# Performance work log

Hardware: AMD Instinct MI355X
Metric: run time of the kernel (lower is better)

## Reference

```python
import jax, jax.numpy as jnp
import numpy as np

EPS = 1e-5

def _bn2d(x, gamma, beta):
    # training-mode BatchNorm2d: stats over (B, T, F) per channel, biased var
    m = x.mean(axis=(0, 2, 3), keepdims=True)
    v = x.var(axis=(0, 2, 3), keepdims=True)
    return (x - m) * jax.lax.rsqrt(v + EPS) * gamma[None, :, None, None] + beta[None, :, None, None]

def _gn1(x, gamma, beta):
    # GroupNorm(num_groups=1) on (B, C, T): stats over (C, T) per sample
    m = x.mean(axis=(1, 2), keepdims=True)
    v = x.var(axis=(1, 2), keepdims=True)
    return (x - m) * jax.lax.rsqrt(v + EPS) * gamma[None, :, None] + beta[None, :, None]

def _nearest(x, size):
    # torch F.interpolate(mode='nearest') on last dim: src = floor(dst * L_in / L_out)
    L = x.shape[-1]
    idx = jnp.floor(jnp.arange(size) * (L / size)).astype(jnp.int32)
    return x[..., idx]


def setup_inputs() -> dict:
    key = jax.random.key(0)
    ks = jax.random.split(key, 16)
    B, Ca, T, Fa = 2, 512, 256, 128
    Tv = 64
    d = {
        "audio": jax.random.normal(ks[0], (B, Ca, T, Fa), dtype=jnp.float32),
        "video_emb": jax.random.normal(ks[1], (B, Ca, Tv), dtype=jnp.float32),
        # value_conv: depthwise 1x1 Conv2d (no bias) + BatchNorm2d
        "value_w": jax.random.normal(ks[2], (Ca,), dtype=jnp.float32) * 0.1 + 1.0,
        "value_gamma": jax.random.normal(ks[3], (Ca,), dtype=jnp.float32) * 0.1 + 1.0,
        "value_beta": jax.random.normal(ks[4], (Ca,), dtype=jnp.float32) * 0.1,
        # gate_conv: depthwise 1x1 Conv2d (no bias) + BatchNorm2d + ReLU
        "gate_w": jax.random.normal(ks[5], (Ca,), dtype=jnp.float32) * 0.1 + 1.0,
        "gate_gamma": jax.random.normal(ks[6], (Ca,), dtype=jnp.float32) * 0.1 + 1.0,
        "gate_beta": jax.random.normal(ks[7], (Ca,), dtype=jnp.float32) * 0.1,
        # attention_conv: depthwise Conv1d (bias) + GroupNorm(1)
        "att_w": jax.random.normal(ks[8], (Ca,), dtype=jnp.float32) * 0.1 + 1.0,
        "att_b": jax.random.normal(ks[9], (Ca,), dtype=jnp.float32) * 0.1,
        "att_gamma": jax.random.normal(ks[10], (Ca,), dtype=jnp.float32) * 0.1 + 1.0,
        "att_beta": jax.random.normal(ks[11], (Ca,), dtype=jnp.float32) * 0.1,
        # resize_conv: depthwise Conv1d (bias) + GroupNorm(1)
        "res_w": jax.random.normal(ks[12], (Ca,), dtype=jnp.float32) * 0.1 + 1.0,
        "res_b": jax.random.normal(ks[13], (Ca,), dtype=jnp.float32) * 0.1,
        "res_gamma": jax.random.normal(ks[14], (Ca,), dtype=jnp.float32) * 0.1 + 1.0,
        "res_beta": jax.random.normal(ks[15], (Ca,), dtype=jnp.float32) * 0.1,
    }
    return d


def reference(audio, video_emb, value_w, value_gamma, value_beta,
              gate_w, gate_gamma, gate_beta,
              att_w, att_b, att_gamma, att_beta,
              res_w, res_b, res_gamma, res_beta):
    T = audio.shape[2]
    # value branch: depthwise 1x1 conv (per-channel scale) + BN
    a_v = _bn2d(audio * value_w[None, :, None, None], value_gamma, value_beta)  # (B,Ca,T,Fa)
    # attention from video: depthwise conv1d + GN(1) + softmax over time + nearest resize
    att = _gn1(video_emb * att_w[None, :, None] + att_b[None, :, None], att_gamma, att_beta)
    att = _nearest(jax.nn.softmax(att, axis=-1), T)  # (B,Ca,T)
    f1 = att[..., None] * a_v
    # gating branch
    vr = _gn1(video_emb * res_w[None, :, None] + res_b[None, :, None], res_gamma, res_beta)
    vi = _nearest(vr, T)[..., None]  # (B,Ca,T,1)
    a_gate = jax.nn.relu(_bn2d(audio * gate_w[None, :, None, None], gate_gamma, gate_beta))
    f2 = a_gate * vi
    return f1 + f2
```

## Files before the change

kernel.cpp:

```cpp
#include <hip/hip_runtime.h>
#include <math.h>

#define EPS 1e-5f

constexpr int B   = 2;
constexpr int Ca  = 512;
constexpr int T   = 256;
constexpr int Fa  = 128;
constexpr int Tv  = 64;
constexpr int CHW = T * Fa;
constexpr int NSTAT = B * CHW;
constexpr int VID_PER_B = Ca * Tv;

__global__ __launch_bounds__(256) void k_stats(
    const float* __restrict__ audio,
    const float* __restrict__ vw, const float* __restrict__ vg, const float* __restrict__ vb,
    const float* __restrict__ gw, const float* __restrict__ gg, const float* __restrict__ gb,
    float* __restrict__ ws)
{
    const int c   = blockIdx.x;
    const int tid = threadIdx.x;
    const float4* a4 = reinterpret_cast<const float4*>(audio);

    float s = 0.f, s2 = 0.f;
    #pragma unroll
    for (int b = 0; b < B; ++b) {
        const float4* base = a4 + ((size_t)(b * Ca + c) * CHW) / 4;
        for (int k = tid; k < CHW / 4; k += 256) {
            float4 v = base[k];
            s  += v.x + v.y + v.z + v.w;
            s2 += v.x * v.x + v.y * v.y + v.z * v.z + v.w * v.w;
        }
    }
    for (int off = 32; off; off >>= 1) {
        s  += __shfl_xor(s,  off);
        s2 += __shfl_xor(s2, off);
    }
    __shared__ float ls[4], ls2[4];
    const int wid = tid >> 6;
    if ((tid & 63) == 0) { ls[wid] = s; ls2[wid] = s2; }
    __syncthreads();
    if (tid == 0) {
        float S  = ls[0]  + ls[1]  + ls[2]  + ls[3];
        float S2 = ls2[0] + ls2[1] + ls2[2] + ls2[3];
        const float inv  = 1.f / (float)NSTAT;
        float mean = S * inv;
        float var  = S2 * inv - mean * mean;

        float w  = vw[c];
        float rs = rsqrtf(w * w * var + EPS);
        float sv = w * rs * vg[c];
        ws[c]        = sv;
        ws[512 + c]  = vb[c] - mean * sv;

        w  = gw[c];
        rs = rsqrtf(w * w * var + EPS);
        float sg = w * rs * gg[c];
        ws[1024 + c] = sg;
        ws[1536 + c] = gb[c] - mean * sg;
    }
}

__global__ __launch_bounds__(1024) void k_video(
    const float* __restrict__ video,
    const float* __restrict__ aw, const float* __restrict__ ab,
    const float* __restrict__ ag, const float* __restrict__ abeta,
    const float* __restrict__ rw, const float* __restrict__ rb,
    const float* __restrict__ rg, const float* __restrict__ rbeta,
    float* __restrict__ att_out, float* __restrict__ vr_out)
{
    const int b   = blockIdx.x;
    const int tid = threadIdx.x;
    const int t   = tid & 63;
    const int cl  = tid >> 6;
    const float* vbase = video + (size_t)b * VID_PER_B;

    float s1a = 0.f, s2a = 0.f, s1r = 0.f, s2r = 0.f;
    #pragma unroll
    for (int i = 0; i < Ca / 16; ++i) {
        const int c = cl + 16 * i;
        float v  = vbase[c * Tv + t];
        float xa = v * aw[c] + ab[c];
        float xr = v * rw[c] + rb[c];
        s1a += xa; s2a += xa * xa;
        s1r += xr; s2r += xr * xr;
    }
    for (int off = 32; off; off >>= 1) {
        s1a += __shfl_xor(s1a, off); s2a += __shfl_xor(s2a, off);
        s1r += __shfl_xor(s1r, off); s2r += __shfl_xor(s2r, off);
    }
    __shared__ float red[4][16];
    __shared__ float stats[4];
    const int wid = tid >> 6;
    if ((tid & 63) == 0) {
        red[0][wid] = s1a; red[1][wid] = s2a;
        red[2][wid] = s1r; red[3][wid] = s2r;
    }
    __syncthreads();
    if (tid == 0) {
        float S1a = 0, S2a = 0, S1r = 0, S2r = 0;
        for (int i = 0; i < 16; ++i) {
            S1a += red[0][i]; S2a += red[1][i];
            S1r += red[2][i]; S2r += red[3][i];
        }
        const float inv = 1.f / (float)VID_PER_B;
        float ma = S1a * inv, va = S2a * inv - ma * ma;
        float mr = S1r * inv, vv = S2r * inv - mr * mr;
        stats[0] = ma; stats[1] = rsqrtf(va + EPS);
        stats[2] = mr; stats[3] = rsqrtf(vv + EPS);
    }
    __syncthreads();
    const float ma = stats[0], rsa = stats[1];
    const float mr = stats[2], rsr = stats[3];

    #pragma unroll
    for (int i = 0; i < Ca / 16; ++i) {
        const int c = cl + 16 * i;
        float v  = vbase[c * Tv + t];
        float xa = (v * aw[c] + ab[c] - ma) * rsa * ag[c] + abeta[c];
        float xr = (v * rw[c] + rb[c] - mr) * rsr * rg[c] + rbeta[c];

        float m = xa;
        for (int off = 32; off; off >>= 1) m = fmaxf(m, __shfl_xor(m, off));
        float e = expf(xa - m);
        float sum = e;
        for (int off = 32; off; off >>= 1) sum += __shfl_xor(sum, off);

        const size_t idx = (size_t)b * VID_PER_B + (size_t)c * Tv + t;
        att_out[idx] = e / sum;
        vr_out[idx]  = xr;
    }
}

__global__ __launch_bounds__(256) void k_fuse(
    const float* __restrict__ audio,
    const float* __restrict__ ws,
    const float* __restrict__ att, const float* __restrict__ vr,
    float* __restrict__ out)
{
    const float4* a4 = reinterpret_cast<const float4*>(audio);
    float4*       o4 = reinterpret_cast<float4*>(out);
    const size_t base = (size_t)blockIdx.x * 1024 + threadIdx.x;

    #pragma unroll
    for (int k = 0; k < 4; ++k) {
        const size_t i  = base + (size_t)k * 256;
        const size_t t4 = i >> 5;
        const int    t  = (int)(t4 & (size_t)(T - 1));
        const size_t bc = t4 >> 8;
        const int    c  = (int)(bc & (size_t)(Ca - 1));

        const float sv = ws[c];
        const float bv = ws[512 + c];
        const float sg = ws[1024 + c];
        const float bg = ws[1536 + c];

        const size_t vidx = bc * Tv + (size_t)(t >> 2);
        const float av = att[vidx];
        const float vv = vr[vidx];

        float4 a = a4[i];
        float4 r;
        r.x = av * (a.x * sv + bv) + fmaxf(a.x * sg + bg, 0.f) * vv;
        r.y = av * (a.y * sv + bv) + fmaxf(a.y * sg + bg, 0.f) * vv;
        r.z = av * (a.z * sv + bv) + fmaxf(a.z * sg + bg, 0.f) * vv;
        r.w = av * (a.w * sv + bv) + fmaxf(a.w * sg + bg, 0.f) * vv;
        o4[i] = r;
    }
}

extern "C" void kernel_launch(void* const* d_in, const int* in_sizes, int n_in,
                              void* d_out, int out_size, void* d_ws, size_t ws_size,
                              hipStream_t stream) {
    const float* audio   = (const float*)d_in[0];
    const float* video   = (const float*)d_in[1];
    const float* value_w = (const float*)d_in[2];
    const float* value_g = (const float*)d_in[3];
    const float* value_b = (const float*)d_in[4];
    const float* gate_w  = (const float*)d_in[5];
    const float* gate_g  = (const float*)d_in[6];
    const float* gate_b  = (const float*)d_in[7];
    const float* att_w   = (const float*)d_in[8];
    const float* att_b   = (const float*)d_in[9];
    const float* att_g   = (const float*)d_in[10];
    const float* att_be  = (const float*)d_in[11];
    const float* res_w   = (const float*)d_in[12];
    const float* res_b   = (const float*)d_in[13];
    const float* res_g   = (const float*)d_in[14];
    const float* res_be  = (const float*)d_in[15];

    float* ws  = (float*)d_ws;
    float* att = ws + 2048;
    float* vrr = att + (size_t)B * VID_PER_B;

    k_stats<<<Ca, 256, 0, stream>>>(audio, value_w, value_g, value_b,
                                    gate_w, gate_g, gate_b, ws);
    k_video<<<B, 1024, 0, stream>>>(video, att_w, att_b, att_g, att_be,
                                    res_w, res_b, res_g, res_be, att, vrr);

    const int total_f4  = B * Ca * T * Fa / 4;
    const int blocks    = total_f4 / 1024;
    k_fuse<<<blocks, 256, 0, stream>>>(audio, ws, att, vrr, (float*)d_out);
}
```

Baseline: 331.1 us.

## Split channel stats across more blocks, move BN finalize to video kernel

The stats kernel now launches 2048 blocks, one per half-channel per batch (16K floats each), instead of 512 blocks that each loop over both batches. Each block writes partial sums, and block 0 of the video kernel combines them into the BN scale and shift coefficients. This raises parallelism for the first reduction pass. The fuse kernel now hoists per-channel coefficients to the block level and uses nontemporal stores for the output. One risk is that the finalize work runs inside only one of the two video blocks.

```diff
diff --git a/kernel.cpp b/kernel.cpp
--- a/kernel.cpp
+++ b/kernel.cpp
@@ -2,6 +2,8 @@
 #include <math.h>
 
 #define EPS 1e-5f
+
+typedef float f32x4 __attribute__((ext_vector_type(4)));
 
 constexpr int B   = 2;
 constexpr int Ca  = 512;
@@ -12,25 +14,25 @@
 constexpr int NSTAT = B * CHW;
 constexpr int VID_PER_B = Ca * Tv;
 
+constexpr int WS_COEF = 0;
+constexpr int WS_PS   = 2048;
+constexpr int WS_PS2  = 4096;
+constexpr int WS_ATT  = 6144;
+constexpr int WS_VR   = WS_ATT + B * VID_PER_B;
+
 __global__ __launch_bounds__(256) void k_stats(
-    const float* __restrict__ audio,
-    const float* __restrict__ vw, const float* __restrict__ vg, const float* __restrict__ vb,
-    const float* __restrict__ gw, const float* __restrict__ gg, const float* __restrict__ gb,
-    float* __restrict__ ws)
+    const float* __restrict__ audio, float* __restrict__ ws)
 {
-    const int c   = blockIdx.x;
+    const int blk = blockIdx.x;
     const int tid = threadIdx.x;
-    const float4* a4 = reinterpret_cast<const float4*>(audio);
+    const f32x4* a4 = reinterpret_cast<const f32x4*>(audio) + (size_t)blk * 4096;
 
     float s = 0.f, s2 = 0.f;
     #pragma unroll
-    for (int b = 0; b < B; ++b) {
-        const float4* base = a4 + ((size_t)(b * Ca + c) * CHW) / 4;
-        for (int k = tid; k < CHW / 4; k += 256) {
-            float4 v = base[k];
-            s  += v.x + v.y + v.z + v.w;
-            s2 += v.x * v.x + v.y * v.y + v.z * v.z + v.w * v.w;
-        }
+    for (int k = 0; k < 16; ++k) {
+        f32x4 v = a4[tid + k * 256];
+        s  += v.x + v.y + v.z + v.w;
+        s2 += v.x * v.x + v.y * v.y + v.z * v.z + v.w * v.w;
     }
     for (int off = 32; off; off >>= 1) {
         s  += __shfl_xor(s,  off);
@@ -41,39 +43,50 @@
     if ((tid & 63) == 0) { ls[wid] = s; ls2[wid] = s2; }
     __syncthreads();
     if (tid == 0) {
-        float S  = ls[0]  + ls[1]  + ls[2]  + ls[3];
-        float S2 = ls2[0] + ls2[1] + ls2[2] + ls2[3];
-        const float inv  = 1.f / (float)NSTAT;
-        float mean = S * inv;
-        float var  = S2 * inv - mean * mean;
-
-        float w  = vw[c];
-        float rs = rsqrtf(w * w * var + EPS);
-        float sv = w * rs * vg[c];
-        ws[c]        = sv;
-        ws[512 + c]  = vb[c] - mean * sv;
-
-        w  = gw[c];
-        rs = rsqrtf(w * w * var + EPS);
-        float sg = w * rs * gg[c];
-        ws[1024 + c] = sg;
-        ws[1536 + c] = gb[c] - mean * sg;
+        ws[WS_PS  + blk] = ls[0]  + ls[1]  + ls[2]  + ls[3];
+        ws[WS_PS2 + blk] = ls2[0] + ls2[1] + ls2[2] + ls2[3];
     }
 }
 
 __global__ __launch_bounds__(1024) void k_video(
     const float* __restrict__ video,
+    const float* __restrict__ vw, const float* __restrict__ vg, const float* __restrict__ vb,
+    const float* __restrict__ gw, const float* __restrict__ gg, const float* __restrict__ gb,
     const float* __restrict__ aw, const float* __restrict__ ab,
     const float* __restrict__ ag, const float* __restrict__ abeta,
     const float* __restrict__ rw, const float* __restrict__ rb,
     const float* __restrict__ rg, const float* __restrict__ rbeta,
-    float* __restrict__ att_out, float* __restrict__ vr_out)
+    float* __restrict__ ws)
 {
     const int b   = blockIdx.x;
     const int tid = threadIdx.x;
-    const int t   = tid & 63;
-    const int cl  = tid >> 6;
+
+    if (b == 0 && tid < Ca) {
+        const int c = tid;
+        const float S  = ws[WS_PS  + c*2] + ws[WS_PS  + c*2 + 1]
+                       + ws[WS_PS  + 1024 + c*2] + ws[WS_PS  + 1024 + c*2 + 1];
+        const float S2 = ws[WS_PS2 + c*2] + ws[WS_PS2 + c*2 + 1]
+                       + ws[WS_PS2 + 1024 + c*2] + ws[WS_PS2 + 1024 + c*2 + 1];
+        const float inv  = 1.f / (float)NSTAT;
+        const float mean = S * inv;
+        const float var  = S2 * inv - mean * mean;
+
+        float w  = vw[c];
+        float sv = w * rsqrtf(w * w * var + EPS) * vg[c];
+        ws[WS_COEF + c]        = sv;
+        ws[WS_COEF + 512 + c]  = vb[c] - mean * sv;
+
+        w = gw[c];
+        float sg = w * rsqrtf(w * w * var + EPS) * gg[c];
+        ws[WS_COEF + 1024 + c] = sg;
+        ws[WS_COEF + 1536 + c] = gb[c] - mean * sg;
+    }
+
+    const int t  = tid & 63;
+    const int cl = tid >> 6;
     const float* vbase = video + (size_t)b * VID_PER_B;
+    float* att_out = ws + WS_ATT;
+    float* vr_out  = ws + WS_VR;
 
     float s1a = 0.f, s2a = 0.f, s1r = 0.f, s2r = 0.f;
     #pragma unroll
@@ -135,37 +148,38 @@
 __global__ __launch_bounds__(256) void k_fuse(
     const float* __restrict__ audio,
     const float* __restrict__ ws,
-    const float* __restrict__ att, const float* __restrict__ vr,
     float* __restrict__ out)
 {
-    const float4* a4 = reinterpret_cast<const float4*>(audio);
-    float4*       o4 = reinterpret_cast<float4*>(out);
-    const size_t base = (size_t)blockIdx.x * 1024 + threadIdx.x;
+    const int blk = blockIdx.x;
+    const int tid = threadIdx.x;
+    const f32x4* a4 = reinterpret_cast<const f32x4*>(audio);
+    f32x4*       o4 = reinterpret_cast<f32x4*>(out);
+
+    const size_t bc = (size_t)(blk >> 3);
+    const int    c  = (int)(bc & (size_t)(Ca - 1));
+    const int    t_base = (blk & 7) * 32;
+
+    const float sv = ws[WS_COEF + c];
+    const float bv = ws[WS_COEF + 512 + c];
+    const float sg = ws[WS_COEF + 1024 + c];
+    const float bg = ws[WS_COEF + 1536 + c];
+    const float* att = ws + WS_ATT + bc * Tv;
+    const float* vr  = ws + WS_VR  + bc * Tv;
 
     #pragma unroll
     for (int k = 0; k < 4; ++k) {
-        const size_t i  = base + (size_t)k * 256;
-        const size_t t4 = i >> 5;
-        const int    t  = (int)(t4 & (size_t)(T - 1));
-        const size_t bc = t4 >> 8;
-        const int    c  = (int)(bc & (size_t)(Ca - 1));
-
-        const float sv = ws[c];
-        const float bv = ws[512 + c];
-        const float sg = ws[1024 + c];
-        const float bg = ws[1536 + c];
-
-        const size_t vidx = bc * Tv + (size_t)(t >> 2);
-        const float av = att[vidx];
-        const float vv = vr[vidx];
-
-        float4 a = a4[i];
-        float4 r;
+        const size_t i = (size_t)blk * 1024 + tid + (size_t)k * 256;
+        const int    t = t_base + k * 8 + (tid >> 5);
+        const float av = att[t >> 2];
+        const float vv = vr[t >> 2];
+
+        f32x4 a = a4[i];
+        f32x4 r;
         r.x = av * (a.x * sv + bv) + fmaxf(a.x * sg + bg, 0.f) * vv;
         r.y = av * (a.y * sv + bv) + fmaxf(a.y * sg + bg, 0.f) * vv;
         r.z = av * (a.z * sv + bv) + fmaxf(a.z * sg + bg, 0.f) * vv;
         r.w = av * (a.w * sv + bv) + fmaxf(a.w * sg + bg, 0.f) * vv;
-        o4[i] = r;
+        __builtin_nontemporal_store(r, &o4[i]);
     }
 }
 
@@ -189,16 +203,14 @@
     const float* res_g   = (const float*)d_in[14];
     const float* res_be  = (const float*)d_in[15];
 
-    float* ws  = (float*)d_ws;
-    float* att = ws + 2048;
-    float* vrr = att + (size_t)B * VID_PER_B;
-
-    k_stats<<<Ca, 256, 0, stream>>>(audio, value_w, value_g, value_b,
-                                    gate_w, gate_g, gate_b, ws);
-    k_video<<<B, 1024, 0, stream>>>(video, att_w, att_b, att_g, att_be,
-                                    res_w, res_b, res_g, res_be, att, vrr);
-
-    const int total_f4  = B * Ca * T * Fa / 4;
-    const int blocks    = total_f4 / 1024;
-    k_fuse<<<blocks, 256, 0, stream>>>(audio, ws, att, vrr, (float*)d_out);
-}
+    float* ws = (float*)d_ws;
+
+    k_stats<<<2048, 256, 0, stream>>>(audio, ws);
+    k_video<<<B, 1024, 0, stream>>>(video,
+                                    value_w, value_g, value_b,
+                                    gate_w, gate_g, gate_b,
+                                    att_w, att_b, att_g, att_be,
+                                    res_w, res_b, res_g, res_be, ws);
+    const int blocks = B * Ca * T * Fa / 4 / 1024;
+    k_fuse<<<blocks, 256, 0, stream>>>(audio, ws, (float*)d_out);
+}
```

Measured after the change: 316.3 us. 4.5% less time.
